# Kernel tuning notes

Measured on AMD Instinct MI355X. Metric: run time of the kernel, lower is better.

## Reference

```python
import jax, jax.numpy as jnp
import numpy as np

DIM = 512
INNER = 512  # heads*dim_head = 8*64
SCALE = 64 ** -0.5  # dim_head^{-0.5}, applied to BOTH q and k as in the source


def setup_inputs() -> dict:
    key = jax.random.key(0)
    k1, k2, k3, k4 = jax.random.split(key, 4)
    x = jax.random.normal(k1, (8, 2048, DIM), dtype=jnp.float32)
    Wqkv = jax.random.normal(k2, (DIM, 3 * INNER), dtype=jnp.float32) * (DIM ** -0.5)
    Wout = jax.random.normal(k3, (INNER, DIM), dtype=jnp.float32) * (INNER ** -0.5)
    bout = jax.random.normal(k4, (DIM,), dtype=jnp.float32) * 0.01
    return {"x": x, "Wqkv": Wqkv, "Wout": Wout, "bout": bout}


def reference(x, Wqkv, Wout, bout):
    # fused QKV projection (no bias)
    qkv = jnp.einsum("bnd,de->bne", x, Wqkv)
    q, k, v = jnp.split(qkv, 3, axis=-1)
    # note: source scales BOTH q and k by dim_head^{-0.5}
    scores = jnp.einsum("bnd,bmd->bnm", q * SCALE, k * SCALE)  # [B,N,N]
    attn = jax.nn.softmax(scores, axis=-1)
    out = jnp.einsum("bnm,bmd->bnd", attn, v)
    # residual add, then output projection (dropout=0.0 -> identity)
    return jnp.einsum("bnd,de->bne", out + x, Wout) + bout
```

## Files before the change

kernel.cpp:

```cpp
#include <hip/hip_runtime.h>
#include <hip/hip_bf16.h>


typedef __attribute__((ext_vector_type(8))) short bf16x8;
typedef __attribute__((ext_vector_type(4))) float f32x4;
typedef __attribute__((ext_vector_type(4))) unsigned short u16x4;

__device__ __forceinline__ unsigned short f2bf(float f) {
  unsigned u = __builtin_bit_cast(unsigned, f);
  u += 0x7fffu + ((u >> 16) & 1u);
  return (unsigned short)(u >> 16);
}
__device__ __forceinline__ float bf2f(unsigned short h) {
  unsigned u = ((unsigned)h) << 16;
  return __builtin_bit_cast(float, u);
}

__device__ __forceinline__ void async16(const unsigned short* g, unsigned short* l) {
  __builtin_amdgcn_global_load_lds(
      (const __attribute__((address_space(1))) unsigned int*)g,
      (__attribute__((address_space(3))) unsigned int*)l, 16, 0, 0);
}

__global__ __launch_bounds__(256) void prep_xw(const float* __restrict__ X,
                                               unsigned short* __restrict__ XB,
                                               const float* __restrict__ W,
                                               unsigned short* __restrict__ WT) {
  const int t = threadIdx.x;
  if (blockIdx.x < 2048) {
    const size_t base = ((size_t)blockIdx.x * 256 + t) * 16;
    f32x4 a0 = *(const f32x4*)&X[base];
    f32x4 a1 = *(const f32x4*)&X[base + 4];
    f32x4 a2 = *(const f32x4*)&X[base + 8];
    f32x4 a3 = *(const f32x4*)&X[base + 12];
    bf16x8 o0, o1;
#pragma unroll
    for (int j = 0; j < 4; ++j) {
      o0[j] = (short)f2bf(a0[j]);
      o0[4 + j] = (short)f2bf(a1[j]);
      o1[j] = (short)f2bf(a2[j]);
      o1[4 + j] = (short)f2bf(a3[j]);
    }
    *(bf16x8*)&XB[base] = o0;
    *(bf16x8*)&XB[base + 8] = o1;
  } else {
    const int bid2 = blockIdx.x - 2048;
    const int c0 = (bid2 % 12) * 128 + (t & 15) * 8;
    const int k0 = (bid2 / 12) * 128 + (t >> 4) * 8;
    float r[8][8];
#pragma unroll
    for (int j = 0; j < 8; ++j) {
      f32x4 lo = *(const f32x4*)&W[(size_t)(k0 + j) * 1536 + c0];
      f32x4 hi = *(const f32x4*)&W[(size_t)(k0 + j) * 1536 + c0 + 4];
#pragma unroll
      for (int q = 0; q < 4; ++q) {
        r[j][q] = lo[q];
        r[j][4 + q] = hi[q];
      }
    }
#pragma unroll
    for (int i = 0; i < 8; ++i) {
      const float scl = (c0 + i < 1024) ? 0.125f : 1.0f;
      bf16x8 o;
#pragma unroll
      for (int j = 0; j < 8; ++j) o[j] = (short)f2bf(r[j][i] * scl);
      *(bf16x8*)&WT[(size_t)(c0 + i) * 512 + k0] = o;
    }
  }
}

__global__ __launch_bounds__(256) void transpose_wout(const float* __restrict__ W,
                                                      unsigned short* __restrict__ WT) {
  const int t = threadIdx.x;
  const int c0 = blockIdx.x * 128 + (t & 15) * 8;
  const int k0 = blockIdx.y * 128 + (t >> 4) * 8;
  float r[8][8];
#pragma unroll
  for (int j = 0; j < 8; ++j) {
    f32x4 lo = *(const f32x4*)&W[(size_t)(k0 + j) * 512 + c0];
    f32x4 hi = *(const f32x4*)&W[(size_t)(k0 + j) * 512 + c0 + 4];
#pragma unroll
    for (int q = 0; q < 4; ++q) {
      r[j][q] = lo[q];
      r[j][4 + q] = hi[q];
    }
  }
#pragma unroll
  for (int i = 0; i < 8; ++i) {
    bf16x8 o;
#pragma unroll
    for (int j = 0; j < 8; ++j) o[j] = (short)f2bf(r[j][i]);
    *(bf16x8*)&WT[(size_t)(c0 + i) * 512 + k0] = o;
  }
}

#define GEMM97_VARS                                            \
  const int tid = threadIdx.x;                                 \
  const int wave = tid >> 6, lane = tid & 63;                  \
  const int wr = wave >> 1, wc = wave & 1;                     \
  const int lg = lane >> 4, ll = lane & 15;                    \
  const int kk = lg * 8;                                       \
  const int srow = wave * 32 + (lane >> 2);                    \
  const int scol = (lane & 3) * 8;

__global__ __launch_bounds__(256, 3) void gemm_qkv97(const unsigned short* __restrict__ XB,
                                                     const unsigned short* __restrict__ WT,
                                                     unsigned short* __restrict__ QKV,
                                                     unsigned short* __restrict__ VT) {
  __shared__ __align__(16) unsigned short Asm[4096];
  __shared__ __align__(16) unsigned short Bsm[4096];
  GEMM97_VARS
  const int bid = blockIdx.x;
  const int qt = bid / 12, nt = bid - qt * 12;
  const unsigned short* Ag = XB + (size_t)(qt * 128) * 512;
  const unsigned short* Bg = WT + (size_t)(nt * 128) * 512;
  f32x4 acc[4][4];
#pragma unroll
  for (int i = 0; i < 4; ++i)
#pragma unroll
    for (int j = 0; j < 4; ++j) acc[i][j] = (f32x4){0.f, 0.f, 0.f, 0.f};
  for (int kt = 0; kt < 512; kt += 32) {
    async16(&Ag[(size_t)srow * 512 + kt + scol], &Asm[wave * 1024]);
    async16(&Ag[(size_t)(srow + 16) * 512 + kt + scol], &Asm[wave * 1024 + 512]);
    async16(&Bg[(size_t)srow * 512 + kt + scol], &Bsm[wave * 1024]);
    async16(&Bg[(size_t)(srow + 16) * 512 + kt + scol], &Bsm[wave * 1024 + 512]);
    __syncthreads();
    bf16x8 af[4], bfr[4];
#pragma unroll
    for (int ai = 0; ai < 4; ++ai) af[ai] = *(const bf16x8*)&Asm[(wr * 64 + ai * 16 + ll) * 32 + kk];
#pragma unroll
    for (int bj = 0; bj < 4; ++bj) bfr[bj] = *(const bf16x8*)&Bsm[(wc * 64 + bj * 16 + ll) * 32 + kk];
#pragma unroll
    for (int ai = 0; ai < 4; ++ai)
#pragma unroll
      for (int bj = 0; bj < 4; ++bj)
        acc[ai][bj] = __builtin_amdgcn_mfma_f32_16x16x32_bf16(af[ai], bfr[bj], acc[ai][bj], 0, 0, 0);
    __syncthreads();
  }
  if (nt < 8) {
#pragma unroll
    for (int ai = 0; ai < 4; ++ai)
#pragma unroll
      for (int bj = 0; bj < 4; ++bj) {
        const int col = nt * 128 + wc * 64 + bj * 16 + ll;
#pragma unroll
        for (int r = 0; r < 4; ++r) {
          const int row = qt * 128 + wr * 64 + ai * 16 + lg * 4 + r;
          QKV[(size_t)row * 1536 + col] = f2bf(acc[ai][bj][r]);
        }
      }
  } else {
#pragma unroll
    for (int ai = 0; ai < 4; ++ai)
#pragma unroll
      for (int bj = 0; bj < 4; ++bj) {
        const int d = (nt - 8) * 128 + wc * 64 + bj * 16 + ll;
        const int row0 = qt * 128 + wr * 64 + ai * 16 + lg * 4;
        u16x4 o;
#pragma unroll
        for (int r = 0; r < 4; ++r) o[r] = f2bf(acc[ai][bj][r]);
        *(u16x4*)&VT[(size_t)d * 16384 + row0] = o;
      }
  }
}

__global__ __launch_bounds__(512) void sgemm256(const unsigned short* __restrict__ QKV,
                                                unsigned short* __restrict__ S,
                                                float* __restrict__ part) {
  __shared__ __align__(16) unsigned short Asm[2][16384];
  __shared__ __align__(16) unsigned short Bsm[2][16384];
  const int tid = threadIdx.x;
  const int wave = tid >> 6, lane = tid & 63;
  const int wr = wave >> 2, wc = wave & 3;
  const int lg = lane >> 4, ll = lane & 15;
  const int bid = blockIdx.x;
  const int b = bid & 7;
  const int idx = bid >> 3;
  const int kvt = idx & 7, qt = idx >> 3;
  const unsigned short* Ag = QKV + ((size_t)b * 2048 + qt * 256) * 1536;
  const unsigned short* Bg = QKV + ((size_t)b * 2048 + kvt * 256) * 1536 + 512;
  const int sr = wave * 8 + (lane >> 3);
  const int sc = (((lane & 7) ^ ((lane >> 3) & 7))) * 8;

  f32x4 acc[8][4];
#pragma unroll
  for (int i = 0; i < 8; ++i)
#pragma unroll
    for (int j = 0; j < 4; ++j) acc[i][j] = (f32x4){0.f, 0.f, 0.f, 0.f};

#define SG_STAGE(BUF, KT)                                                              \
  _Pragma("unroll") for (int i = 0; i < 4; ++i) {                                      \
    async16(&Ag[(size_t)(i * 64 + sr) * 1536 + (KT) + sc], &Asm[BUF][(i * 64 + wave * 8) * 64]); \
    async16(&Bg[(size_t)(i * 64 + sr) * 1536 + (KT) + sc], &Bsm[BUF][(i * 64 + wave * 8) * 64]); \
  }

  SG_STAGE(0, 0)
  int cur = 0;
  __syncthreads();
  for (int kt = 0; kt < 512; kt += 64) {
    if (kt + 64 < 512) {
      if (cur) { SG_STAGE(0, kt + 64) } else { SG_STAGE(1, kt + 64) }
    }
#pragma unroll
    for (int half = 0; half < 2; ++half) {
      const int kb = (((half * 4 + lg) ^ (ll & 7))) * 8;
      bf16x8 af[8], bf4[4];
#pragma unroll
      for (int ai = 0; ai < 8; ++ai)
        af[ai] = *(const bf16x8*)&Asm[cur][(wr * 128 + ai * 16 + ll) * 64 + kb];
#pragma unroll
      for (int bj = 0; bj < 4; ++bj)
        bf4[bj] = *(const bf16x8*)&Bsm[cur][(wc * 64 + bj * 16 + ll) * 64 + kb];
#pragma unroll
      for (int ai = 0; ai < 8; ++ai)
#pragma unroll
        for (int bj = 0; bj < 4; ++bj)
          acc[ai][bj] = __builtin_amdgcn_mfma_f32_16x16x32_bf16(af[ai], bf4[bj], acc[ai][bj], 0, 0, 0);
    }
    __syncthreads();
    cur ^= 1;
  }
#undef SG_STAGE

#pragma unroll
  for (int ai = 0; ai < 8; ++ai)
#pragma unroll
    for (int bj = 0; bj < 4; ++bj)
#pragma unroll
      for (int r = 0; r < 4; ++r) acc[ai][bj][r] = __expf(acc[ai][bj][r]);

#pragma unroll
  for (int ai = 0; ai < 8; ++ai)
#pragma unroll
    for (int r = 0; r < 4; ++r) {
      float se = (acc[ai][0][r] + acc[ai][1][r]) + (acc[ai][2][r] + acc[ai][3][r]);
      se += __shfl_xor(se, 1);
      se += __shfl_xor(se, 2);
      se += __shfl_xor(se, 4);
      se += __shfl_xor(se, 8);
      if (ll == 0) {
        const size_t rowg = (size_t)b * 2048 + qt * 256 + wr * 128 + ai * 16 + lg * 4 + r;
        part[rowg * 32 + kvt * 4 + wc] = se;
      }
    }

  unsigned short* Sg = S + (size_t)b * 2048 * 2048;
#pragma unroll
  for (int ai = 0; ai < 8; ++ai)
#pragma unroll
    for (int bj = 0; bj < 4; ++bj) {
      const int col = kvt * 256 + wc * 64 + bj * 16 + ll;
#pragma unroll
      for (int r = 0; r < 4; ++r) {
        const int row = qt * 256 + wr * 128 + ai * 16 + lg * 4 + r;
        Sg[(size_t)row * 2048 + col] = f2bf(acc[ai][bj][r]);
      }
    }
}

__global__ __launch_bounds__(256, 3) void pvgemm97(const unsigned short* __restrict__ S,
                                                   const unsigned short* __restrict__ VT,
                                                   const float* __restrict__ X,
                                                   const float* __restrict__ part,
                                                   unsigned short* __restrict__ RES) {
  __shared__ __align__(16) unsigned short Asm[2][8192];
  __shared__ __align__(16) unsigned short Bsm[2][8192];
  __shared__ float invl_s[128];
  const int tid = threadIdx.x;
  const int wave = tid >> 6, lane = tid & 63;
  const int wr = wave >> 1, wc = wave & 1;
  const int lg = lane >> 4, ll = lane & 15;
  const int bid = blockIdx.x;
  const int b = bid & 7;
  const int idx = bid >> 3;
  const int dt = idx & 3, qt = idx >> 2;
  const unsigned short* Ag = S + (size_t)b * 2048 * 2048 + (size_t)(qt * 128) * 2048;
  const unsigned short* Bg = VT + (size_t)(dt * 128) * 16384 + (size_t)b * 2048;
  const int sr = wave * 32 + (lane >> 3);
  const int sc = (((lane & 7) ^ ((lane >> 3) & 7))) * 8;

  f32x4 acc[4][4];
#pragma unroll
  for (int i = 0; i < 4; ++i)
#pragma unroll
    for (int j = 0; j < 4; ++j) acc[i][j] = (f32x4){0.f, 0.f, 0.f, 0.f};

#define PV_STAGE(BUF, KT)                                                                   \
  _Pragma("unroll") for (int i = 0; i < 4; ++i) {                                           \
    async16(&Ag[(size_t)(sr + i * 8) * 2048 + (KT) + sc], &Asm[BUF][(wave * 32 + i * 8) * 64]);  \
    async16(&Bg[(size_t)(sr + i * 8) * 16384 + (KT) + sc], &Bsm[BUF][(wave * 32 + i * 8) * 64]); \
  }

  PV_STAGE(0, 0)
  if (tid < 128) {
    const size_t rowg = (size_t)b * 2048 + qt * 128 + tid;
    float l = 0.f;
#pragma unroll
    for (int t = 0; t < 8; ++t) {
      f32x4 v = *(const f32x4*)&part[rowg * 32 + t * 4];
      l += (v[0] + v[1]) + (v[2] + v[3]);
    }
    invl_s[tid] = 1.0f / l;
  }
  int cur = 0;
  __syncthreads();
  for (int kt = 0; kt < 2048; kt += 64) {
    if (kt + 64 < 2048) {
      if (cur) { PV_STAGE(0, kt + 64) } else { PV_STAGE(1, kt + 64) }
    }
#pragma unroll
    for (int half = 0; half < 2; ++half) {
      const int kb = (((half * 4 + lg) ^ (ll & 7))) * 8;
      bf16x8 af[4], bf4[4];
#pragma unroll
      for (int ai = 0; ai < 4; ++ai)
        af[ai] = *(const bf16x8*)&Asm[cur][(wr * 64 + ai * 16 + ll) * 64 + kb];
#pragma unroll
      for (int bj = 0; bj < 4; ++bj)
        bf4[bj] = *(const bf16x8*)&Bsm[cur][(wc * 64 + bj * 16 + ll) * 64 + kb];
#pragma unroll
      for (int ai = 0; ai < 4; ++ai)
#pragma unroll
        for (int bj = 0; bj < 4; ++bj)
          acc[ai][bj] = __builtin_amdgcn_mfma_f32_16x16x32_bf16(af[ai], bf4[bj], acc[ai][bj], 0, 0, 0);
    }
    __syncthreads();
    cur ^= 1;
  }
#undef PV_STAGE

  const int rowbase = b * 2048 + qt * 128 + wr * 64;
  float il[4][4];
#pragma unroll
  for (int ai = 0; ai < 4; ++ai)
#pragma unroll
    for (int r = 0; r < 4; ++r) il[ai][r] = invl_s[wr * 64 + ai * 16 + lg * 4 + r];
#pragma unroll
  for (int ai = 0; ai < 4; ++ai)
#pragma unroll
    for (int bj = 0; bj < 4; ++bj) {
      const int col = dt * 128 + wc * 64 + bj * 16 + ll;
#pragma unroll
      for (int r = 0; r < 4; ++r) {
        const size_t row = (size_t)rowbase + ai * 16 + lg * 4 + r;
        const float val = acc[ai][bj][r] * il[ai][r] + X[row * 512 + col];
        RES[row * 1536 + 1024 + col] = f2bf(val);
      }
    }
}

__global__ __launch_bounds__(256, 3) void gemm_out97(const unsigned short* __restrict__ A,
                                                     const unsigned short* __restrict__ WT,
                                                     const float* __restrict__ bias,
                                                     float* __restrict__ OUT) {
  __shared__ __align__(16) unsigned short Asm[4096];
  __shared__ __align__(16) unsigned short Bsm[4096];
  GEMM97_VARS
  const int bid = blockIdx.x;
  const int dt = bid & 3, qt = bid >> 2;
  const unsigned short* Ag = A + (size_t)(qt * 128) * 1536 + 1024;
  const unsigned short* Bg = WT + (size_t)(dt * 128) * 512;
  f32x4 acc[4][4];
#pragma unroll
  for (int i = 0; i < 4; ++i)
#pragma unroll
    for (int j = 0; j < 4; ++j) acc[i][j] = (f32x4){0.f, 0.f, 0.f, 0.f};
  for (int kt = 0; kt < 512; kt += 32) {
    async16(&Ag[(size_t)srow * 1536 + kt + scol], &Asm[wave * 1024]);
    async16(&Ag[(size_t)(srow + 16) * 1536 + kt + scol], &Asm[wave * 1024 + 512]);
    async16(&Bg[(size_t)srow * 512 + kt + scol], &Bsm[wave * 1024]);
    async16(&Bg[(size_t)(srow + 16) * 512 + kt + scol], &Bsm[wave * 1024 + 512]);
    __syncthreads();
    bf16x8 af[4], bfr[4];
#pragma unroll
    for (int ai = 0; ai < 4; ++ai) af[ai] = *(const bf16x8*)&Asm[(wr * 64 + ai * 16 + ll) * 32 + kk];
#pragma unroll
    for (int bj = 0; bj < 4; ++bj) bfr[bj] = *(const bf16x8*)&Bsm[(wc * 64 + bj * 16 + ll) * 32 + kk];
#pragma unroll
    for (int ai = 0; ai < 4; ++ai)
#pragma unroll
      for (int bj = 0; bj < 4; ++bj)
        acc[ai][bj] = __builtin_amdgcn_mfma_f32_16x16x32_bf16(af[ai], bfr[bj], acc[ai][bj], 0, 0, 0);
    __syncthreads();
  }
#pragma unroll
  for (int ai = 0; ai < 4; ++ai)
#pragma unroll
    for (int bj = 0; bj < 4; ++bj) {
      const int col = dt * 128 + wc * 64 + bj * 16 + ll;
      const float bv = bias[col];
#pragma unroll
      for (int r = 0; r < 4; ++r) {
        const int row = qt * 128 + wr * 64 + ai * 16 + lg * 4 + r;
        OUT[(size_t)row * 512 + col] = acc[ai][bj][r] + bv;
      }
    }
}

extern "C" void kernel_launch(void* const* d_in, const int* in_sizes, int n_in,
                              void* d_out, int out_size, void* d_ws, size_t ws_size,
                              hipStream_t stream) {
  const float* x = (const float*)d_in[0];
  const float* Wqkv = (const float*)d_in[1];
  const float* Wout = (const float*)d_in[2];
  const float* bout = (const float*)d_in[3];
  float* out = (float*)d_out;

  unsigned short* qkvb = (unsigned short*)d_ws;
  unsigned short* VT = qkvb + (size_t)16384 * 1536;
  unsigned short* S = VT + (size_t)512 * 16384;
  unsigned short* xb = S;
  unsigned short* WT = S + (size_t)16384 * 512;
  float* part = out;

  prep_xw<<<2096, 256, 0, stream>>>(x, xb, Wqkv, WT);
  gemm_qkv97<<<1536, 256, 0, stream>>>(xb, WT, qkvb, VT);
  sgemm256<<<512, 512, 0, stream>>>(qkvb, S, part);
  pvgemm97<<<512, 256, 0, stream>>>(S, VT, x, part, qkvb);
  transpose_wout<<<dim3(4, 4), 256, 0, stream>>>(Wout, (unsigned short*)S);
  gemm_out97<<<512, 256, 0, stream>>>(qkvb, (unsigned short*)S, bout, out);
}
```

Baseline: 169.1 us.

## Process two KV tiles per block in score GEMM to overlap epilogue with loads

The score GEMM kernel now has each block compute two adjacent 256-wide KV tiles in one continuous 16-step pipeline, halving the grid from 512 to 256 blocks. The prefetch for the second tile is issued before the first tile's exp/sum/store epilogue, so the epilogue can overlap with the next loads and the pipeline prologue is paid once per two tiles. The trade-off is 256 blocks of 512 threads on a 256-CU part, which leaves roughly one block per CU. The unchanged Q tile is also re-streamed rather than reused.

Result: slower. 221.5 us (+31.0%).

```diff
diff --git a/kernel.cpp b/kernel.cpp
--- a/kernel.cpp
+++ b/kernel.cpp
@@ -176,9 +176,10 @@
   const int bid = blockIdx.x;
   const int b = bid & 7;
   const int idx = bid >> 3;
-  const int kvt = idx & 7, qt = idx >> 3;
+  const int kvp = idx & 3, qt = idx >> 2;
   const unsigned short* Ag = QKV + ((size_t)b * 2048 + qt * 256) * 1536;
-  const unsigned short* Bg = QKV + ((size_t)b * 2048 + kvt * 256) * 1536 + 512;
+  const unsigned short* Bg0 = QKV + ((size_t)b * 2048 + (kvp * 2 + 0) * 256) * 1536 + 512;
+  const unsigned short* Bg1 = QKV + ((size_t)b * 2048 + (kvp * 2 + 1) * 256) * 1536 + 512;
   const int sr = wave * 8 + (lane >> 3);
   const int sc = (((lane & 7) ^ ((lane >> 3) & 7))) * 8;
 
@@ -188,18 +189,49 @@
 #pragma unroll
     for (int j = 0; j < 4; ++j) acc[i][j] = (f32x4){0.f, 0.f, 0.f, 0.f};
 
-#define SG_STAGE(BUF, KT)                                                              \
+#define SG_STAGE(BUF, BGP, KT)                                                         \
   _Pragma("unroll") for (int i = 0; i < 4; ++i) {                                      \
-    async16(&Ag[(size_t)(i * 64 + sr) * 1536 + (KT) + sc], &Asm[BUF][(i * 64 + wave * 8) * 64]); \
-    async16(&Bg[(size_t)(i * 64 + sr) * 1536 + (KT) + sc], &Bsm[BUF][(i * 64 + wave * 8) * 64]); \
-  }
-
-  SG_STAGE(0, 0)
+    async16(&Ag[(size_t)(i * 64 + sr) * 1536 + (KT) + sc], &Asm[BUF][(i * 64 + wave * 8) * 64]);  \
+    async16(&(BGP)[(size_t)(i * 64 + sr) * 1536 + (KT) + sc], &Bsm[BUF][(i * 64 + wave * 8) * 64]); \
+  }
+
+#define SG_EPILOGUE(KVT)                                                               \
+  _Pragma("unroll") for (int ai = 0; ai < 8; ++ai)                                     \
+  _Pragma("unroll") for (int bj = 0; bj < 4; ++bj)                                     \
+  _Pragma("unroll") for (int r = 0; r < 4; ++r) acc[ai][bj][r] = __expf(acc[ai][bj][r]); \
+  _Pragma("unroll") for (int ai = 0; ai < 8; ++ai)                                     \
+  _Pragma("unroll") for (int r = 0; r < 4; ++r) {                                      \
+    float se = (acc[ai][0][r] + acc[ai][1][r]) + (acc[ai][2][r] + acc[ai][3][r]);      \
+    se += __shfl_xor(se, 1);                                                           \
+    se += __shfl_xor(se, 2);                                                           \
+    se += __shfl_xor(se, 4);                                                           \
+    se += __shfl_xor(se, 8);                                                           \
+    if (ll == 0) {                                                                     \
+      const size_t rowg = (size_t)b * 2048 + qt * 256 + wr * 128 + ai * 16 + lg * 4 + r; \
+      part[rowg * 32 + (KVT) * 4 + wc] = se;                                           \
+    }                                                                                  \
+  }                                                                                    \
+  {                                                                                    \
+    unsigned short* Sg = S + (size_t)b * 2048 * 2048;                                  \
+    _Pragma("unroll") for (int ai = 0; ai < 8; ++ai)                                   \
+    _Pragma("unroll") for (int bj = 0; bj < 4; ++bj) {                                 \
+      const int col = (KVT) * 256 + wc * 64 + bj * 16 + ll;                            \
+      _Pragma("unroll") for (int r = 0; r < 4; ++r) {                                  \
+        const int row = qt * 256 + wr * 128 + ai * 16 + lg * 4 + r;                    \
+        Sg[(size_t)row * 2048 + col] = f2bf(acc[ai][bj][r]);                           \
+      }                                                                                \
+    }                                                                                  \
+  }
+
+  SG_STAGE(0, Bg0, 0)
   int cur = 0;
   __syncthreads();
-  for (int kt = 0; kt < 512; kt += 64) {
-    if (kt + 64 < 512) {
-      if (cur) { SG_STAGE(0, kt + 64) } else { SG_STAGE(1, kt + 64) }
+  for (int tt = 0; tt < 16; ++tt) {
+    if (tt < 15) {
+      const int ntt = tt + 1;
+      const unsigned short* nbg = (ntt >= 8) ? Bg1 : Bg0;
+      const int nkt = (ntt & 7) * 64;
+      if (cur) { SG_STAGE(0, nbg, nkt) } else { SG_STAGE(1, nbg, nkt) }
     }
 #pragma unroll
     for (int half = 0; half < 2; ++half) {
@@ -219,43 +251,17 @@
     }
     __syncthreads();
     cur ^= 1;
-  }
+    if (tt == 7) {
+      SG_EPILOGUE(kvp * 2)
+#pragma unroll
+      for (int i = 0; i < 8; ++i)
+#pragma unroll
+        for (int j = 0; j < 4; ++j) acc[i][j] = (f32x4){0.f, 0.f, 0.f, 0.f};
+    }
+  }
+  SG_EPILOGUE(kvp * 2 + 1)
 #undef SG_STAGE
-
-#pragma unroll
-  for (int ai = 0; ai < 8; ++ai)
-#pragma unroll
-    for (int bj = 0; bj < 4; ++bj)
-#pragma unroll
-      for (int r = 0; r < 4; ++r) acc[ai][bj][r] = __expf(acc[ai][bj][r]);
-
-#pragma unroll
-  for (int ai = 0; ai < 8; ++ai)
-#pragma unroll
-    for (int r = 0; r < 4; ++r) {
-      float se = (acc[ai][0][r] + acc[ai][1][r]) + (acc[ai][2][r] + acc[ai][3][r]);
-      se += __shfl_xor(se, 1);
-      se += __shfl_xor(se, 2);
-      se += __shfl_xor(se, 4);
-      se += __shfl_xor(se, 8);
-      if (ll == 0) {
-        const size_t rowg = (size_t)b * 2048 + qt * 256 + wr * 128 + ai * 16 + lg * 4 + r;
-        part[rowg * 32 + kvt * 4 + wc] = se;
-      }
-    }
-
-  unsigned short* Sg = S + (size_t)b * 2048 * 2048;
-#pragma unroll
-  for (int ai = 0; ai < 8; ++ai)
-#pragma unroll
-    for (int bj = 0; bj < 4; ++bj) {
-      const int col = kvt * 256 + wc * 64 + bj * 16 + ll;
-#pragma unroll
-      for (int r = 0; r < 4; ++r) {
-        const int row = qt * 256 + wr * 128 + ai * 16 + lg * 4 + r;
-        Sg[(size_t)row * 2048 + col] = f2bf(acc[ai][bj][r]);
-      }
-    }
+#undef SG_EPILOGUE
 }
 
 __global__ __launch_bounds__(256, 3) void pvgemm97(const unsigned short* __restrict__ S,
@@ -415,7 +421,7 @@
 
   prep_xw<<<2096, 256, 0, stream>>>(x, xb, Wqkv, WT);
   gemm_qkv97<<<1536, 256, 0, stream>>>(xb, WT, qkvb, VT);
-  sgemm256<<<512, 512, 0, stream>>>(qkvb, S, part);
+  sgemm256<<<256, 512, 0, stream>>>(qkvb, S, part);
   pvgemm97<<<512, 256, 0, stream>>>(S, VT, x, part, qkvb);
   transpose_wout<<<dim3(4, 4), 256, 0, stream>>>(Wout, (unsigned short*)S);
   gemm_out97<<<512, 256, 0, stream>>>(qkvb, (unsigned short*)S, bout, out);
```
